# Kernel optimization log

Hardware: AMD Instinct MI355X
Metric: run time of the kernel (lower is better)

## Reference

```python
import jax, jax.numpy as jnp
import numpy as np

B, T = 1, 2048
N_HEAD = 16
N_KV_HEAD = 16
N_EMBD = 1024
HEAD_DIM = N_EMBD // N_HEAD  # 64
HD8 = HEAD_DIM // 8          # 8 octonion blocks per head
EPS_RMS = 1e-6


def qconj(q):
    return q * jnp.array([1.0, -1.0, -1.0, -1.0], dtype=q.dtype)


def qmul(q1, q2):
    # Hamilton product, (...,4) x (...,4) -> (...,4)
    w1, x1, y1, z1 = (q1[..., 0], q1[..., 1], q1[..., 2], q1[..., 3])
    w2, x2, y2, z2 = (q2[..., 0], q2[..., 1], q2[..., 2], q2[..., 3])
    return jnp.stack([
        w1 * w2 - x1 * x2 - y1 * y2 - z1 * z2,
        w1 * x2 + x1 * w2 + y1 * z2 - z1 * y2,
        w1 * y2 - x1 * z2 + y1 * w2 + z1 * x2,
        w1 * z2 + x1 * y2 - y1 * x2 + z1 * w2,
    ], axis=-1)


def omul(o1, o2):
    # Cayley-Dickson octonion product, (...,8)
    a, b = o1[..., :4], o1[..., 4:]
    c, d = o2[..., :4], o2[..., 4:]
    first = qmul(a, c) - qmul(qconj(d), b)
    second = qmul(d, a) + qmul(b, qconj(c))
    return jnp.concatenate([first, second], axis=-1)


def oconj(o):
    return jnp.concatenate([qconj(o[..., :4]), -o[..., 4:]], axis=-1)


# Octonion multiplication structure constants: omul(x, y)[k] = x[a] y[p] C[a,p,k]
_EYE8 = jnp.eye(8, dtype=jnp.float32)
C_OCT = jax.vmap(lambda ei: jax.vmap(lambda ej: omul(ei, ej))(_EYE8))(_EYE8)  # (8,8,8)
# Trilinear tensor for omul(omul(q, kc), v):  T3[a,p,q,k] = sum_e C[a,p,e] C[e,q,k]
T3 = jnp.einsum('ape,eqk->apqk', C_OCT, C_OCT)  # (8,8,8,8)


def apply_rotary_emb(x, cos, sin):
    # x: (B, T, H, hd); cos/sin: (1, T, 1, hd//2)
    d = x.shape[-1] // 2
    x1, x2 = x[..., :d], x[..., d:]
    y1 = x1 * cos + x2 * sin
    y2 = x2 * cos - x1 * sin
    return jnp.concatenate([y1, y2], axis=-1)


def rms_norm(x):
    return x * jax.lax.rsqrt(jnp.mean(x * x, axis=-1, keepdims=True) + EPS_RMS)


def setup_inputs() -> dict:
    key = jax.random.key(0)
    ks = jax.random.split(key, 7)
    x = jax.random.normal(ks[0], (B, T, N_EMBD), dtype=jnp.float32)
    cos = jax.random.uniform(ks[1], (1, T, 1, HEAD_DIM // 2), dtype=jnp.float32)
    sin = jax.random.uniform(ks[2], (1, T, 1, HEAD_DIM // 2), dtype=jnp.float32)
    s = 0.02
    Wq = jax.random.normal(ks[3], (N_HEAD * HEAD_DIM, N_EMBD), dtype=jnp.float32) * s
    Wk = jax.random.normal(ks[4], (N_KV_HEAD * HEAD_DIM, N_EMBD), dtype=jnp.float32) * s
    Wv = jax.random.normal(ks[5], (N_KV_HEAD * HEAD_DIM, N_EMBD), dtype=jnp.float32) * s
    Wo = jax.random.normal(ks[6], (N_EMBD, N_EMBD), dtype=jnp.float32) * s
    return {"x": x, "cos": cos, "sin": sin, "Wq": Wq, "Wk": Wk, "Wv": Wv, "Wo": Wo}


def reference(x, cos, sin, Wq, Wk, Wv, Wo):
    Bx, Tx, Cx = x.shape
    q = (x @ Wq.T).reshape(Bx, Tx, N_HEAD, HEAD_DIM)
    k = (x @ Wk.T).reshape(Bx, Tx, N_KV_HEAD, HEAD_DIM)
    v = (x @ Wv.T).reshape(Bx, Tx, N_KV_HEAD, HEAD_DIM)
    q = rms_norm(apply_rotary_emb(q, cos, sin))
    k = rms_norm(apply_rotary_emb(k, cos, sin))
    q = q.transpose(0, 2, 1, 3)  # (B,H,T,hd)
    k = k.transpose(0, 2, 1, 3)
    v = v.transpose(0, 2, 1, 3)

    q_o = q.reshape(Bx, N_HEAD, Tx, HD8, 8)
    k_o = k.reshape(Bx, N_KV_HEAD, Tx, HD8, 8)
    v_o = v.reshape(Bx, N_KV_HEAD, Tx, HD8, 8)
    # F.normalize(p=2, dim=-1): divide by max(||.||, 1e-12)
    k_o = k_o / jnp.maximum(jnp.linalg.norm(k_o, axis=-1, keepdims=True), 1e-12)

    # Scores use the (pre-octonion-normalized) rotary+rms k
    scores = jnp.einsum('bhid,bhjd->bhij', q, k) * (HEAD_DIM ** -0.5)
    mask = jnp.tril(jnp.ones((Tx, Tx), dtype=bool))
    scores = jnp.where(mask, scores, -jnp.inf)
    probs = jax.nn.softmax(scores, axis=-1)  # (B,H,Tq,Tk)

    # y_i = sum_j p_ij * omul(omul(q_i, oconj(k_j)), v_j)
    # omul is bilinear, so pull the j-sum inside:
    # y_i[k] = q_i[a] * T3[a,p,c,k] * (sum_j p_ij kc_j[p] v_j[c])
    kc = oconj(k_o)                                              # (B,H,Tk,M,8)
    KV = jnp.einsum('bhjmp,bhjmq->bhjmpq', kc, v_o)              # (B,H,Tk,M,8,8)
    Z = jnp.einsum('bhij,bhjmpq->bhimpq', probs, KV)             # (B,H,Tq,M,8,8)
    y_o = jnp.einsum('bhima,apqk,bhimpq->bhimk', q_o, T3, Z)     # (B,H,Tq,M,8)

    y = y_o.reshape(Bx, N_HEAD, Tx, HEAD_DIM).transpose(0, 2, 1, 3).reshape(Bx, Tx, Cx)
    return y @ Wo.T
```

## Files before the change

kernel.cpp:

```cpp
#include <hip/hip_runtime.h>

typedef unsigned short u16;
typedef unsigned int u32;

#define T_SEQ 2048
#define NHEAD 16
#define HDIM 64
#define CDIM 1024
#define W_HSTR (512*2048)
#define Z_HSTR (2048*512)
#define P_HSTR 2228224
#define P_TILE 16384

#define SGBITS 0xB2D8741EACC66A00ULL

#define EXP2C 0.18033688011112042f

typedef _Float16 f16x8 __attribute__((ext_vector_type(8)));
typedef float f32x4 __attribute__((ext_vector_type(4)));

__device__ __forceinline__ float h2f(u16 u) { _Float16 h; __builtin_memcpy(&h, &u, 2); return (float)h; }
__device__ __forceinline__ u16 f2h(float f) { _Float16 h = (_Float16)f; u16 u; __builtin_memcpy(&u, &h, 2); return u; }
__device__ __forceinline__ u32 pk(float a, float b) { return (u32)f2h(a) | ((u32)f2h(b) << 16); }

__device__ __forceinline__ void gload16(const u16* g, u16* l) {
    __builtin_amdgcn_global_load_lds((const __attribute__((address_space(1))) u32*)g,
                                     (__attribute__((address_space(3))) u32*)l, 16, 0, 0);
}

template<bool F16OUT>
__device__ __forceinline__ void hgemm_tile(const u16* __restrict__ At, int lda,
                                           const u16* __restrict__ Bt, int ldb, int K,
                                           float* __restrict__ Cf, u16* __restrict__ Ch,
                                           int ldc, float scale, u16* As, u16* Bs) {
    int t = threadIdx.x;
    int wave = t >> 6, l = t & 63;
    int wm = wave & 1, wn = wave >> 1;
    int quad = l >> 4, lr = l & 15;
    f32x4 acc[4][4];
#pragma unroll
    for (int i = 0; i < 4; ++i)
#pragma unroll
        for (int j = 0; j < 4; ++j) acc[i][j] = (f32x4){0.f, 0.f, 0.f, 0.f};
    int acol = quad * 8;
    for (int k0 = 0; k0 < K; k0 += 64) {
#pragma unroll
        for (int j = 0; j < 4; ++j) {
            int d = wave * 4 + j;
            int kb = d >> 3, seg = d & 7;
            size_t roff = (size_t)(seg * 16 + lr);
            int coff = k0 + kb * 32 + acol;
            gload16(At + roff * lda + coff, As + d * 512);
            gload16(Bt + roff * ldb + coff, Bs + d * 512);
        }
        __syncthreads();
#pragma unroll
        for (int kb = 0; kb < 2; ++kb) {
            f16x8 af[4], bf[4];
#pragma unroll
            for (int mi = 0; mi < 4; ++mi) af[mi] = *(const f16x8*)&As[(kb * 8 + wm * 4 + mi) * 512 + l * 8];
#pragma unroll
            for (int ni = 0; ni < 4; ++ni) bf[ni] = *(const f16x8*)&Bs[(kb * 8 + wn * 4 + ni) * 512 + l * 8];
#pragma unroll
            for (int mi = 0; mi < 4; ++mi)
#pragma unroll
                for (int ni = 0; ni < 4; ++ni)
                    acc[mi][ni] = __builtin_amdgcn_mfma_f32_16x16x32_f16(af[mi], bf[ni], acc[mi][ni], 0, 0, 0);
        }
        __syncthreads();
    }
#pragma unroll
    for (int mi = 0; mi < 4; ++mi)
#pragma unroll
        for (int ni = 0; ni < 4; ++ni)
#pragma unroll
            for (int rr = 0; rr < 4; ++rr) {
                int gr = wm * 64 + mi * 16 + quad * 4 + rr;
                int gc = wn * 64 + ni * 16 + lr;
                float v = acc[mi][ni][rr] * scale;
                if (F16OUT) Ch[(size_t)gr * ldc + gc] = f2h(v);
                else Cf[(size_t)gr * ldc + gc] = v;
            }
}

__global__ __launch_bounds__(256) void hgemm_f32(const u16* __restrict__ A, int lda,
                                                 const u16* __restrict__ B, int ldb,
                                                 float* __restrict__ C, int ldc, int K) {
    __shared__ u16 As[8192], Bs[8192];
    int bm = blockIdx.y * 128, bn = blockIdx.x * 128;
    hgemm_tile<false>(A + (size_t)bm * lda, lda, B + (size_t)bn * ldb, ldb, K,
                      C + (size_t)bm * ldc + bn, nullptr, ldc, 1.f, As, Bs);
}

__global__ __launch_bounds__(256) void hgemm_f16(const u16* __restrict__ A, int lda,
                                                 const u16* __restrict__ B, int ldb,
                                                 u16* __restrict__ C, int ldc, int K) {
    __shared__ u16 As[8192], Bs[8192];
    int bm = blockIdx.y * 128, bn = blockIdx.x * 128;
    hgemm_tile<true>(A + (size_t)bm * lda, lda, B + (size_t)bn * ldb, ldb, K,
                     nullptr, C + (size_t)bm * ldc + bn, ldc, 1.f, As, Bs);
}

__global__ __launch_bounds__(256) void qk_exp_p(const u16* __restrict__ q16,
                                                const u16* __restrict__ k16,
                                                u16* __restrict__ P) {
    __shared__ u16 Pt[128 * 144];
    int idx = blockIdx.x;
    int h = idx & 15;
    int tt = idx >> 4;
    int rb = 0;
    while ((rb + 1) * (rb + 2) / 2 <= tt) rb++;
    int cb = tt - rb * (rb + 1) / 2;
    int t = threadIdx.x;
    int wave = t >> 6, l = t & 63;
    int wm = wave & 1, wn = wave >> 1;
    int quad = l >> 4, lr = l & 15;

    const u16* qbase = q16 + (size_t)(rb * 128 + wm * 64 + lr) * CDIM + h * HDIM + quad * 8;
    const u16* kbase = k16 + (size_t)(cb * 128 + wn * 64 + lr) * CDIM + h * HDIM + quad * 8;
    f16x8 qa[4][2], kf[4][2];
#pragma unroll
    for (int mi = 0; mi < 4; ++mi)
#pragma unroll
        for (int kb = 0; kb < 2; ++kb)
            qa[mi][kb] = *(const f16x8*)(qbase + (size_t)(mi * 16) * CDIM + kb * 32);
#pragma unroll
    for (int ni = 0; ni < 4; ++ni)
#pragma unroll
        for (int kb = 0; kb < 2; ++kb)
            kf[ni][kb] = *(const f16x8*)(kbase + (size_t)(ni * 16) * CDIM + kb * 32);

    f32x4 s[4][4];
#pragma unroll
    for (int mi = 0; mi < 4; ++mi)
#pragma unroll
        for (int ni = 0; ni < 4; ++ni) s[mi][ni] = (f32x4){0.f, 0.f, 0.f, 0.f};
#pragma unroll
    for (int kb = 0; kb < 2; ++kb)
#pragma unroll
        for (int mi = 0; mi < 4; ++mi)
#pragma unroll
            for (int ni = 0; ni < 4; ++ni)
                s[mi][ni] = __builtin_amdgcn_mfma_f32_16x16x32_f16(qa[mi][kb], kf[ni][kb], s[mi][ni], 0, 0, 0);

#pragma unroll
    for (int mi = 0; mi < 4; ++mi) {
        int row = wm * 64 + mi * 16 + quad * 4;
#pragma unroll
        for (int ni = 0; ni < 4; ++ni) {
            int col = wn * 64 + ni * 16 + lr;
#pragma unroll
            for (int rr = 0; rr < 4; ++rr) {
                bool valid = (cb < rb) | (col <= row + rr);
                float p = valid ? __builtin_amdgcn_exp2f(s[mi][ni][rr] * EXP2C - 12.f) : 0.f;
                Pt[(row + rr) * 144 + col] = f2h(p);
            }
        }
    }
    __syncthreads();
    u16* Pg = P + (size_t)h * P_HSTR + (size_t)tt * P_TILE;
#pragma unroll
    for (int i = 0; i < 8; ++i) {
        int c = i * 256 + t;
        int row = c >> 4, cw = c & 15;
        uint4 v = *(const uint4*)&Pt[row * 144 + cw * 8];
        *(uint4*)(Pg + row * 128 + cw * 8) = v;
    }
}

__global__ __launch_bounds__(512, 4) void pw_gemm(const u16* __restrict__ P,
                                                  const u16* __restrict__ W,
                                                  u16* __restrict__ Z,
                                                  float* __restrict__ lbuf) {
    __shared__ u16 As[8192], Bs[8192];
    int b = blockIdx.x;
    int jp = b >> 6;
    int i6 = b & 63;
    int h = ((i6 & 7) << 1) | ((i6 >> 3) & 1);
    int nq = i6 >> 4;
    const u16* Bt = W + (size_t)h * W_HSTR + (size_t)(nq * 128) * T_SEQ;
    u16* Zb = Z + (size_t)h * Z_HSTR;
    int t = threadIdx.x;
    int wave = t >> 6, l = t & 63;
    int wr = wave >> 1, wc = wave & 1;
    int quad = l >> 4, lr = l & 15;
    int acol = quad * 8;
    f16x8 ones;
#pragma unroll
    for (int j = 0; j < 8; ++j) ones[j] = (_Float16)1.0f;

#pragma unroll 1
    for (int jobi = 0; jobi < 2; ++jobi) {
        int rb = jobi ? jp : 15 - jp;
        int K = (rb + 1) * 128;
        const u16* Ph = P + (size_t)h * P_HSTR + (size_t)(rb * (rb + 1) / 2) * P_TILE;
        f32x4 acc[2][4];
        f32x4 accl[2];
#pragma unroll
        for (int mi = 0; mi < 2; ++mi) {
            accl[mi] = (f32x4){0.f, 0.f, 0.f, 0.f};
#pragma unroll
            for (int ni = 0; ni < 4; ++ni) acc[mi][ni] = (f32x4){0.f, 0.f, 0.f, 0.f};
        }
        for (int k0 = 0; k0 < K; k0 += 64) {
            const u16* At = Ph + (size_t)(k0 >> 7) * P_TILE + (k0 & 64);
#pragma unroll
            for (int j = 0; j < 2; ++j) {
                int d = wave * 2 + j;
                int kb = d >> 3, seg = d & 7;
                size_t roff = (size_t)(seg * 16 + lr);
                gload16(At + roff * 128 + kb * 32 + acol, As + d * 512);
                gload16(Bt + roff * T_SEQ + k0 + kb * 32 + acol, Bs + d * 512);
            }
            __syncthreads();
#pragma unroll
            for (int kb = 0; kb < 2; ++kb) {
                f16x8 af[2], bf[4];
#pragma unroll
                for (int mi = 0; mi < 2; ++mi) af[mi] = *(const f16x8*)&As[(kb * 8 + wr * 2 + mi) * 512 + l * 8];
#pragma unroll
                for (int ni = 0; ni < 4; ++ni) bf[ni] = *(const f16x8*)&Bs[(kb * 8 + wc * 4 + ni) * 512 + l * 8];
#pragma unroll
                for (int mi = 0; mi < 2; ++mi) {
#pragma unroll
                    for (int ni = 0; ni < 4; ++ni)
                        acc[mi][ni] = __builtin_amdgcn_mfma_f32_16x16x32_f16(af[mi], bf[ni], acc[mi][ni], 0, 0, 0);
                    if (nq == 0 && wc == 0)
                        accl[mi] = __builtin_amdgcn_mfma_f32_16x16x32_f16(af[mi], ones, accl[mi], 0, 0, 0);
                }
            }
            __syncthreads();
        }
#pragma unroll
        for (int mi = 0; mi < 2; ++mi)
#pragma unroll
            for (int rr = 0; rr < 4; ++rr) {
                int row = rb * 128 + wr * 32 + mi * 16 + quad * 4 + rr;
#pragma unroll
                for (int ni = 0; ni < 4; ++ni) {
                    int col = nq * 128 + wc * 64 + ni * 16 + lr;
                    Zb[(size_t)row * 512 + col] = f2h(acc[mi][ni][rr]);
                }
            }
        if (nq == 0 && wc == 0 && lr == 0) {
#pragma unroll
            for (int mi = 0; mi < 2; ++mi) {
                int row = rb * 128 + wr * 32 + mi * 16 + quad * 4;
                *(f32x4*)(lbuf + h * T_SEQ + row) = accl[mi];
            }
        }
    }
}

__global__ __launch_bounds__(256) void cvt5(const float* __restrict__ x, const float* __restrict__ wq,
                                            const float* __restrict__ wk, const float* __restrict__ wv,
                                            const float* __restrict__ wo,
                                            u16* __restrict__ x16, u16* __restrict__ w16) {
    int z = blockIdx.y;
    size_t base = ((size_t)blockIdx.x * 256 + threadIdx.x) * 8;
    const float* src;
    u16* dst;
    size_t cnt;
    if (z == 0) { src = x; dst = x16; cnt = 2097152; }
    else if (z == 1) { src = wq; dst = w16; cnt = 1048576; }
    else if (z == 2) { src = wk; dst = w16 + 1048576; cnt = 1048576; }
    else if (z == 3) { src = wv; dst = w16 + 2097152; cnt = 1048576; }
    else { src = wo; dst = w16 + 3145728; cnt = 1048576; }
    if (base >= cnt) return;
    float4 f0 = *(const float4*)(src + base);
    float4 f1 = *(const float4*)(src + base + 4);
    uint4 o;
    o.x = pk(f0.x, f0.y); o.y = pk(f0.z, f0.w); o.z = pk(f1.x, f1.y); o.w = pk(f1.z, f1.w);
    *(uint4*)(dst + base) = o;
}

__global__ __launch_bounds__(256) void prep_rope(const u16* __restrict__ qkv,
                                                 u16* __restrict__ q16, u16* __restrict__ k16,
                                                 float* __restrict__ kc,
                                                 const float* __restrict__ cosb, const float* __restrict__ sinb) {
    int wave = threadIdx.x >> 6, lane = threadIdx.x & 63;
    int idx = blockIdx.x * 4 + wave;
    int t = idx >> 4, h = idx & 15;
    int d = lane & 31;
    float cs = cosb[t * 32 + d];
    float sn = sinb[t * 32 + d];
    size_t b3 = (size_t)t * 3072 + h * HDIM;
    size_t b1 = (size_t)t * CDIM + h * HDIM;

    float xq = h2f(qkv[b3 + lane]);
    float oq = __shfl(xq, lane ^ 32);
    float rq = (lane < 32) ? fmaf(xq, cs, oq * sn) : fmaf(xq, cs, -oq * sn);
    float ssq = rq * rq;
#pragma unroll
    for (int m = 1; m < 64; m <<= 1) ssq += __shfl_xor(ssq, m);
    rq *= rsqrtf(ssq * (1.f / 64.f) + 1e-6f);
    q16[b1 + lane] = f2h(rq);

    float xk = h2f(qkv[b3 + 1024 + lane]);
    float ok = __shfl(xk, lane ^ 32);
    float rk = (lane < 32) ? fmaf(xk, cs, ok * sn) : fmaf(xk, cs, -ok * sn);
    float ssk = rk * rk;
#pragma unroll
    for (int m = 1; m < 64; m <<= 1) ssk += __shfl_xor(ssk, m);
    rk *= rsqrtf(ssk * (1.f / 64.f) + 1e-6f);
    k16[b1 + lane] = f2h(rk);

    float s8 = rk * rk;
    s8 += __shfl_xor(s8, 1); s8 += __shfl_xor(s8, 2); s8 += __shfl_xor(s8, 4);
    float sc2 = 1.f / fmaxf(sqrtf(s8), 1e-12f);
    float kcv = rk * sc2;
    if (lane & 7) kcv = -kcv;
    kc[b1 + lane] = kcv;
}

__global__ __launch_bounds__(256) void w_pre(const float* __restrict__ kc, const u16* __restrict__ qkv,
                                             u16* __restrict__ W) {
    __shared__ float kcs[64][65];
    __shared__ float vs[64][65];
    int h = blockIdx.y;
    int j0 = blockIdx.x * 64;
    int t = threadIdx.x;
    int r = t >> 2, cq = (t & 3) * 16;
    const float* kp = kc + (size_t)(j0 + r) * CDIM + h * HDIM + cq;
    const u16* vp = qkv + (size_t)(j0 + r) * 3072 + 2048 + h * HDIM + cq;
#pragma unroll
    for (int u4 = 0; u4 < 4; ++u4) {
        float4 a = *(const float4*)(kp + u4 * 4);
        ushort4 b = *(const ushort4*)(vp + u4 * 4);
        kcs[r][cq + u4 * 4 + 0] = a.x; kcs[r][cq + u4 * 4 + 1] = a.y;
        kcs[r][cq + u4 * 4 + 2] = a.z; kcs[r][cq + u4 * 4 + 3] = a.w;
        vs[r][cq + u4 * 4 + 0] = h2f(b.x); vs[r][cq + u4 * 4 + 1] = h2f(b.y);
        vs[r][cq + u4 * 4 + 2] = h2f(b.z); vs[r][cq + u4 * 4 + 3] = h2f(b.w);
    }
    __syncthreads();
    int j = t & 63, g = t >> 6;
    u16* Wp = W + (size_t)h * W_HSTR + j0 + j;
    for (int ae = g * 16; ae < g * 16 + 16; ++ae) {
        int a = ae >> 3, e = ae & 7;
        u32 mask = 0;
#pragma unroll
        for (int qq = 0; qq < 8; ++qq) {
            int p = a ^ e ^ qq;
            u32 bit = (u32)(((SGBITS >> (a * 8 + p)) ^ (SGBITS >> ((e ^ qq) * 8 + qq))) & 1ULL);
            mask |= bit << qq;
        }
#pragma unroll
        for (int m = 0; m < 8; ++m) {
            float w = 0.f;
#pragma unroll
            for (int qq = 0; qq < 8; ++qq) {
                float t1 = kcs[j][m * 8 + (a ^ e ^ qq)] * vs[j][m * 8 + qq];
                w = ((mask >> qq) & 1) ? (w - t1) : (w + t1);
            }
            Wp[(size_t)(m * 64 + ae) * T_SEQ] = f2h(w);
        }
    }
}

__global__ __launch_bounds__(256) void contract_y(const u16* __restrict__ q16, const u16* __restrict__ Z,
                                                  const float* __restrict__ lbuf, u16* __restrict__ y16) {
    __shared__ u16 zb[4][512];
    int wave = threadIdx.x >> 6, lane = threadIdx.x & 63;
    int idx = blockIdx.x * 4 + wave;
    int i = idx >> 4, h = idx & 15;
    uint4 zv = *(const uint4*)(Z + (size_t)h * Z_HSTR + (size_t)i * 512 + lane * 8);
    *(uint4*)&zb[wave][lane * 8] = zv;
    int m = lane >> 3, e = lane & 7;
    const u16* qp = q16 + (size_t)i * CDIM + h * HDIM + m * 8;
    uint4 qb = *(const uint4*)qp;
    float qv[8];
    qv[0] = h2f(qb.x & 0xffff); qv[1] = h2f(qb.x >> 16);
    qv[2] = h2f(qb.y & 0xffff); qv[3] = h2f(qb.y >> 16);
    qv[4] = h2f(qb.z & 0xffff); qv[5] = h2f(qb.z >> 16);
    qv[6] = h2f(qb.w & 0xffff); qv[7] = h2f(qb.w >> 16);
    float linv = 1.f / lbuf[h * T_SEQ + i];
    __syncthreads();
    float acc = 0.f;
#pragma unroll
    for (int a = 0; a < 8; ++a) acc = fmaf(qv[a], h2f(zb[wave][m * 64 + a * 8 + e]), acc);
    y16[(size_t)i * CDIM + h * HDIM + lane] = f2h(acc * linv);
}

extern "C" void kernel_launch(void* const* d_in, const int* in_sizes, int n_in,
                              void* d_out, int out_size, void* d_ws, size_t ws_size,
                              hipStream_t stream) {
    const float* x = (const float*)d_in[0];
    const float* cosb = (const float*)d_in[1];
    const float* sinb = (const float*)d_in[2];
    const float* Wq = (const float*)d_in[3];
    const float* Wk = (const float*)d_in[4];
    const float* Wv = (const float*)d_in[5];
    const float* Wo = (const float*)d_in[6];
    float* out = (float*)d_out;
    char* base = (char*)d_ws;
    u16* qkv16 = (u16*)base;
    float* kc = (float*)(base + 12582912);
    u16* x16 = (u16*)(base + 20971520);
    u16* w16 = (u16*)(base + 25165824);
    u16* q16 = (u16*)(base + 33554432);
    u16* k16 = (u16*)(base + 37748736);
    u16* y16 = (u16*)(base + 41943040);
    u16* W = (u16*)(base + 46137344);
    u16* Z = (u16*)(base + 79691776);
    float* lbuf = (float*)(base + 113246208);
    u16* Pbuf = (u16*)(base + 113377280);

    cvt5<<<dim3(1024, 5), 256, 0, stream>>>(x, Wq, Wk, Wv, Wo, x16, w16);
    hgemm_f16<<<dim3(24, 16), 256, 0, stream>>>(x16, CDIM, w16, CDIM, qkv16, 3072, CDIM);
    prep_rope<<<T_SEQ * NHEAD / 4, 256, 0, stream>>>(qkv16, q16, k16, kc, cosb, sinb);
    qk_exp_p<<<16 * 136, 256, 0, stream>>>(q16, k16, Pbuf);
    w_pre<<<dim3(32, 16), 256, 0, stream>>>(kc, qkv16, W);
    pw_gemm<<<512, 512, 0, stream>>>(Pbuf, W, Z, lbuf);
    contract_y<<<NHEAD * T_SEQ / 4, 256, 0, stream>>>(q16, Z, lbuf, y16);
    hgemm_f32<<<dim3(8, 16), 256, 0, stream>>>(y16, CDIM, w16 + 3145728, CDIM, out, CDIM, CDIM);
}
```

Baseline: 282.5 us.

## Double-buffer LDS tiles in pw_gemm to overlap global loads with MFMA

The pw_gemm K-loop now keeps two LDS buffers for the A and B tiles. The next K-step is issued with async global_load_lds into the idle buffer while MFMAs run on the current one. The two __syncthreads per iteration become one explicit vmcnt wait plus one barrier. The aim is to hide global-load latency behind compute, at the cost of doubling shared memory per block, which may lower how many blocks fit on each CU.

```diff
diff --git a/kernel.cpp b/kernel.cpp
--- a/kernel.cpp
+++ b/kernel.cpp
@@ -15,6 +15,8 @@
 #define SGBITS 0xB2D8741EACC66A00ULL
 
 #define EXP2C 0.18033688011112042f
+
+#define WAITCNT_VM0 0x0F70
 
 typedef _Float16 f16x8 __attribute__((ext_vector_type(8)));
 typedef float f32x4 __attribute__((ext_vector_type(4)));
@@ -172,7 +174,7 @@
                                                   const u16* __restrict__ W,
                                                   u16* __restrict__ Z,
                                                   float* __restrict__ lbuf) {
-    __shared__ u16 As[8192], Bs[8192];
+    __shared__ u16 As[2][8192], Bs[2][8192];
     int b = blockIdx.x;
     int jp = b >> 6;
     int i6 = b & 63;
@@ -185,6 +187,10 @@
     int wr = wave >> 1, wc = wave & 1;
     int quad = l >> 4, lr = l & 15;
     int acol = quad * 8;
+    int d0 = wave * 2, d1 = wave * 2 + 1;
+    int kq0 = d0 >> 3, sg0 = d0 & 7;
+    int kq1 = d1 >> 3, sg1 = d1 & 7;
+    size_t ro0 = (size_t)(sg0 * 16 + lr), ro1 = (size_t)(sg1 * 16 + lr);
     f16x8 ones;
 #pragma unroll
     for (int j = 0; j < 8; ++j) ones[j] = (_Float16)1.0f;
@@ -192,7 +198,7 @@
 #pragma unroll 1
     for (int jobi = 0; jobi < 2; ++jobi) {
         int rb = jobi ? jp : 15 - jp;
-        int K = (rb + 1) * 128;
+        int nsteps = (rb + 1) * 2;
         const u16* Ph = P + (size_t)h * P_HSTR + (size_t)(rb * (rb + 1) / 2) * P_TILE;
         f32x4 acc[2][4];
         f32x4 accl[2];
@@ -202,24 +208,27 @@
 #pragma unroll
             for (int ni = 0; ni < 4; ++ni) acc[mi][ni] = (f32x4){0.f, 0.f, 0.f, 0.f};
         }
-        for (int k0 = 0; k0 < K; k0 += 64) {
+        auto stage = [&](int k0, int buf) {
             const u16* At = Ph + (size_t)(k0 >> 7) * P_TILE + (k0 & 64);
-#pragma unroll
-            for (int j = 0; j < 2; ++j) {
-                int d = wave * 2 + j;
-                int kb = d >> 3, seg = d & 7;
-                size_t roff = (size_t)(seg * 16 + lr);
-                gload16(At + roff * 128 + kb * 32 + acol, As + d * 512);
-                gload16(Bt + roff * T_SEQ + k0 + kb * 32 + acol, Bs + d * 512);
-            }
-            __syncthreads();
+            gload16(At + ro0 * 128 + kq0 * 32 + acol, &As[buf][d0 * 512]);
+            gload16(Bt + ro0 * T_SEQ + k0 + kq0 * 32 + acol, &Bs[buf][d0 * 512]);
+            gload16(At + ro1 * 128 + kq1 * 32 + acol, &As[buf][d1 * 512]);
+            gload16(Bt + ro1 * T_SEQ + k0 + kq1 * 32 + acol, &Bs[buf][d1 * 512]);
+        };
+        stage(0, 0);
+        __builtin_amdgcn_s_waitcnt(WAITCNT_VM0);
+        __builtin_amdgcn_s_barrier();
+        int cur = 0;
+#pragma unroll 1
+        for (int s = 0; s < nsteps; ++s) {
+            if (s + 1 < nsteps) stage((s + 1) * 64, cur ^ 1);
 #pragma unroll
             for (int kb = 0; kb < 2; ++kb) {
                 f16x8 af[2], bf[4];
 #pragma unroll
-                for (int mi = 0; mi < 2; ++mi) af[mi] = *(const f16x8*)&As[(kb * 8 + wr * 2 + mi) * 512 + l * 8];
-#pragma unroll
-                for (int ni = 0; ni < 4; ++ni) bf[ni] = *(const f16x8*)&Bs[(kb * 8 + wc * 4 + ni) * 512 + l * 8];
+                for (int mi = 0; mi < 2; ++mi) af[mi] = *(const f16x8*)&As[cur][(kb * 8 + wr * 2 + mi) * 512 + l * 8];
+#pragma unroll
+                for (int ni = 0; ni < 4; ++ni) bf[ni] = *(const f16x8*)&Bs[cur][(kb * 8 + wc * 4 + ni) * 512 + l * 8];
 #pragma unroll
                 for (int mi = 0; mi < 2; ++mi) {
 #pragma unroll
@@ -229,7 +238,9 @@
                         accl[mi] = __builtin_amdgcn_mfma_f32_16x16x32_f16(af[mi], ones, accl[mi], 0, 0, 0);
                 }
             }
-            __syncthreads();
+            __builtin_amdgcn_s_waitcnt(WAITCNT_VM0);
+            __builtin_amdgcn_s_barrier();
+            cur ^= 1;
         }
 #pragma unroll
         for (int mi = 0; mi < 2; ++mi)
```

Measured after the change: 283.3 us. Within noise of the previous version (+0.3%).
